# Kernel tuning notes

Measured on AMD Instinct MI355X. Metric: run time of the kernel, lower is better.

The kernel has to match this reference:

```python
import jax, jax.numpy as jnp
import jax.scipy.linalg as jsl
import numpy as np

EPS = 1e-6          # config.eps
MIN_EIG = 1e-4      # config.min_eigenvalue
B, N, K = 2, 2048, 3


def _so3_generators():
    # standard so(3) basis: [G_c]_{kl} = -eps_{ckl}
    G = np.zeros((3, 3, 3), np.float32)
    G[0, 1, 2] = -1.0; G[0, 2, 1] = 1.0
    G[1, 0, 2] = 1.0;  G[1, 2, 0] = -1.0
    G[2, 0, 1] = -1.0; G[2, 1, 0] = 1.0
    return jnp.asarray(G)


def _spd(key, b, n, k):
    # well-conditioned SPD covariances (as a real model would produce)
    A = jax.random.normal(key, (b, n, k, k), jnp.float32)
    return jnp.einsum('bnkl,bnml->bnkm', A, A) / k + 0.5 * jnp.eye(k, dtype=jnp.float32)


def setup_inputs() -> dict:
    key = jax.random.key(0)
    k0, k1, k2, k3 = jax.random.split(key, 4)
    Sigma_prior = _spd(k0, B, N, K)
    Sigma_q = _spd(k1, B, N, K)
    phi = jax.random.normal(k2, (B, N, K), jnp.float32)          # gauge field, C == K == 3
    beta = jax.random.uniform(k3, (B, N, N), jnp.float32) / N    # attention-like weights, rows O(1)
    return {
        'Sigma_prior': Sigma_prior,
        'Sigma_q': Sigma_q,
        'phi': phi,
        'beta': beta,
        'generators': _so3_generators(),
    }


def _batched_expm(mats):
    # mats: (B, N, K, K) -> elementwise matrix exponential
    b, n, k, _ = mats.shape
    return jax.vmap(jsl.expm)(mats.reshape(-1, k, k)).reshape(b, n, k, k)


def reference(Sigma_prior, Sigma_q, phi, beta, generators):
    b, n, k, _ = Sigma_prior.shape
    I = jnp.eye(k, dtype=Sigma_prior.dtype)

    # precisions (regularized inverses)
    Lambda_p = jnp.linalg.inv(Sigma_prior + EPS * I)   # (B,N,K,K)
    Lambda_q = jnp.linalg.inv(Sigma_q + EPS * I)       # (B,N,K,K)

    # gauge transport Omega_ij = e^{phi_i} e^{-phi_j}
    phi_mat = jnp.einsum('bnc,ckl->bnkl', phi, generators)
    exp_phi = _batched_expm(phi_mat)
    exp_neg_phi = _batched_expm(-phi_mat)
    Omega = jnp.einsum('bikl,bjlm->bijkm', exp_phi, exp_neg_phi)   # (B,N,N,K,K)

    # transported neighbor precision: Omega Lambda_q Omega^T
    Lt = jnp.einsum('bijkl,bjlm,bijnm->bijkn', Omega, Lambda_q, Omega)

    # incoming social term: sum_j beta_ij * Lt_ij
    M_in = jnp.einsum('bij,bijkl->bikl', beta, Lt)

    # outgoing recoil: (sum_j beta_ji) * Lambda_q_i
    M_out = beta.sum(axis=1)[..., None, None] * Lambda_q

    M = Lambda_p + M_in + M_out
    M = 0.5 * (M + jnp.swapaxes(M, -1, -2))

    # eigenvalue floor + inverse via eigh
    w, V = jnp.linalg.eigh(M)
    w = jnp.maximum(w, MIN_EIG)
    M_pd = jnp.einsum('bnkl,bnl,bnml->bnkm', V, w, V)
    M_inv = jnp.einsum('bnkl,bnl,bnml->bnkm', V, 1.0 / w, V)
    return M_pd, M_inv
```

## Files before the change

### kernel.cpp

```cpp
#include <hip/hip_runtime.h>
#include <math.h>

#define EPS_REG 1e-6f
#define MIN_EIG_F 1e-4f
#define RB 8


__device__ __forceinline__ void sym_inv3(const float m[3][3], float o[3][3]) {
    float c00 = m[1][1]*m[2][2] - m[1][2]*m[2][1];
    float c01 = m[1][2]*m[2][0] - m[1][0]*m[2][2];
    float c02 = m[1][0]*m[2][1] - m[1][1]*m[2][0];
    float det = m[0][0]*c00 + m[0][1]*c01 + m[0][2]*c02;
    float inv = 1.0f / det;
    o[0][0] = c00*inv;
    o[1][0] = c01*inv;
    o[2][0] = c02*inv;
    o[0][1] = (m[0][2]*m[2][1]-m[0][1]*m[2][2])*inv;
    o[1][1] = (m[0][0]*m[2][2]-m[0][2]*m[2][0])*inv;
    o[2][1] = (m[0][1]*m[2][0]-m[0][0]*m[2][1])*inv;
    o[0][2] = (m[0][1]*m[1][2]-m[0][2]*m[1][1])*inv;
    o[1][2] = (m[0][2]*m[1][0]-m[0][0]*m[1][2])*inv;
    o[2][2] = (m[0][0]*m[1][1]-m[0][1]*m[1][0])*inv;
}

__device__ __forceinline__ void rodrigues(float w0, float w1, float w2, float R[3][3]) {
    float th2 = w0*w0 + w1*w1 + w2*w2;
    float th = sqrtf(th2);
    float a, b;
    if (th < 1e-4f) { a = 1.0f - th2*(1.0f/6.0f); b = 0.5f - th2*(1.0f/24.0f); }
    else            { a = sinf(th)/th;            b = (1.0f - cosf(th))/th2; }
    R[0][0] = 1.0f + b*(w0*w0 - th2); R[0][1] = -a*w2 + b*w0*w1;        R[0][2] =  a*w1 + b*w0*w2;
    R[1][0] =  a*w2 + b*w0*w1;        R[1][1] = 1.0f + b*(w1*w1 - th2); R[1][2] = -a*w0 + b*w1*w2;
    R[2][0] = -a*w1 + b*w0*w2;        R[2][1] =  a*w0 + b*w1*w2;        R[2][2] = 1.0f + b*(w2*w2 - th2);
}

__device__ __forceinline__ void jrot(float A[3][3], float V[3][3], int p, int q) {
    float apq = A[p][q];
    if (fabsf(apq) < 1e-20f) return;
    float theta = (A[q][q] - A[p][p]) / (2.0f * apq);
    float t = 1.0f / (fabsf(theta) + sqrtf(1.0f + theta*theta));
    if (theta < 0.0f) t = -t;
    float c = 1.0f / sqrtf(1.0f + t*t);
    float s = t * c;
    int r = 3 - p - q;
    float apq_t = t*apq;
    A[p][p] -= apq_t;
    A[q][q] += apq_t;
    A[p][q] = 0.0f; A[q][p] = 0.0f;
    float arp = A[r][p], arq = A[r][q];
    A[r][p] = c*arp - s*arq; A[p][r] = A[r][p];
    A[r][q] = s*arp + c*arq; A[q][r] = A[r][q];
    #pragma unroll
    for (int k = 0; k < 3; k++) {
        float vkp = V[k][p], vkq = V[k][q];
        V[k][p] = c*vkp - s*vkq;
        V[k][q] = s*vkp + c*vkq;
    }
}

__global__ __launch_bounds__(64) void precompute_S_kernel(
        const float* __restrict__ Sq,
        const float* __restrict__ phi,
        float* __restrict__ S,
        int BN) {
    __shared__ float sq_s[576];
    __shared__ float ph_s[192];
    __shared__ float so_s[384];
    int tid = threadIdx.x;
    int p0 = blockIdx.x * 64;

    const float4* src = (const float4*)(Sq + (size_t)p0 * 9);
    #pragma unroll
    for (int i = tid; i < 144; i += 64) ((float4*)sq_s)[i] = src[i];
    const float4* psrc = (const float4*)(phi + (size_t)p0 * 3);
    if (tid < 48) ((float4*)ph_s)[tid] = psrc[tid];
    __syncthreads();

    float m[3][3], lq[3][3];
    #pragma unroll
    for (int i = 0; i < 3; i++)
        #pragma unroll
        for (int j = 0; j < 3; j++) m[i][j] = sq_s[tid*9 + i*3 + j];
    m[0][0] += EPS_REG; m[1][1] += EPS_REG; m[2][2] += EPS_REG;
    sym_inv3(m, lq);

    float R[3][3];
    rodrigues(ph_s[tid*3], ph_s[tid*3+1], ph_s[tid*3+2], R);

    float U[3][3];
    #pragma unroll
    for (int i = 0; i < 3; i++)
        #pragma unroll
        for (int j = 0; j < 3; j++)
            U[i][j] = lq[i][0]*R[0][j] + lq[i][1]*R[1][j] + lq[i][2]*R[2][j];
    float s00 = R[0][0]*U[0][0] + R[1][0]*U[1][0] + R[2][0]*U[2][0];
    float s01 = R[0][0]*U[0][1] + R[1][0]*U[1][1] + R[2][0]*U[2][1];
    float s02 = R[0][0]*U[0][2] + R[1][0]*U[1][2] + R[2][0]*U[2][2];
    float s11 = R[0][1]*U[0][1] + R[1][1]*U[1][1] + R[2][1]*U[2][1];
    float s12 = R[0][1]*U[0][2] + R[1][1]*U[1][2] + R[2][1]*U[2][2];
    float s22 = R[0][2]*U[0][2] + R[1][2]*U[1][2] + R[2][2]*U[2][2];
    so_s[tid*6+0]=s00; so_s[tid*6+1]=s01; so_s[tid*6+2]=s02;
    so_s[tid*6+3]=s11; so_s[tid*6+4]=s12; so_s[tid*6+5]=s22;
    __syncthreads();
    float4* dst = (float4*)(S + (size_t)p0 * 6);
    #pragma unroll
    for (int i = tid; i < 96; i += 64) dst[i] = ((float4*)so_s)[i];
}

__global__ __launch_bounds__(256) void fused_beta_kernel(
        const float* __restrict__ beta,
        const float* __restrict__ S,
        float* __restrict__ T,
        float* __restrict__ partial,
        int B, int N) {
    int tid = threadIdx.x;
    int grow0 = blockIdx.x * RB;
    int b = grow0 / N;
    int chunksPerB = N / RB;
    int chunk = (grow0 - b * N) / RB;
    const float* sb = S + (size_t)b * N * 6;

    float acc[RB][6];
    #pragma unroll
    for (int r = 0; r < RB; r++)
        #pragma unroll
        for (int c = 0; c < 6; c++) acc[r][c] = 0.0f;

    int jtiles = N / 1024;
    for (int jt = 0; jt < jtiles; jt++) {
        int c0 = jt * 1024 + 4 * tid;
        float4 s4[6];
        const float4* sp = (const float4*)(sb + (size_t)c0 * 6);
        #pragma unroll
        for (int u = 0; u < 6; u++) s4[u] = sp[u];
        const float* sv = (const float*)s4;

        float csum0 = 0.f, csum1 = 0.f, csum2 = 0.f, csum3 = 0.f;
        #pragma unroll
        for (int r = 0; r < RB; r++) {
            float4 w4 = *(const float4*)(beta + (size_t)(grow0 + r) * N + c0);
            csum0 += w4.x; csum1 += w4.y; csum2 += w4.z; csum3 += w4.w;
            #pragma unroll
            for (int c = 0; c < 6; c++) {
                acc[r][c] += w4.x * sv[0*6 + c];
                acc[r][c] += w4.y * sv[1*6 + c];
                acc[r][c] += w4.z * sv[2*6 + c];
                acc[r][c] += w4.w * sv[3*6 + c];
            }
        }
        *(float4*)(partial + ((size_t)b * chunksPerB + chunk) * N + c0) =
            make_float4(csum0, csum1, csum2, csum3);
    }

    __shared__ float red[256][49];
    __shared__ float red2[4][48];
    #pragma unroll
    for (int r = 0; r < RB; r++)
        #pragma unroll
        for (int c = 0; c < 6; c++)
            red[tid][r * 6 + c] = acc[r][c];
    __syncthreads();
    if (tid < 192) {
        int v = tid % 48, grp = tid / 48;
        float s = 0.0f;
        #pragma unroll 8
        for (int r = 0; r < 64; r++) s += red[grp * 64 + r][v];
        red2[grp][v] = s;
    }
    __syncthreads();
    if (tid < 48) {
        float v = red2[0][tid] + red2[1][tid] + red2[2][tid] + red2[3][tid];
        T[(size_t)grow0 * 6 + tid] = v;
    }
}

__global__ __launch_bounds__(256) void finalize_kernel(
        const float* __restrict__ Sp,
        const float* __restrict__ Sq,
        const float* __restrict__ phi,
        const float* __restrict__ T,
        const float* __restrict__ partial,
        float* __restrict__ out,
        int B, int N) {
    int tid  = threadIdx.x;
    int lane = tid & 63;
    int sub  = tid >> 6;
    int p0   = blockIdx.x * 64;
    int BN   = B * N;
    int b    = p0 / N;
    int i0   = p0 - b * N;
    int chunks = N / RB;

    __shared__ float redc[4][64];
    __shared__ float sp_s[576], sq_s[576], ph_s[192], t_s[384];
    __shared__ float o1_s[576], o2_s[576];

    int cpg = chunks / 4;
    float csp = 0.0f;
    const float* pp = partial + ((size_t)b * chunks + sub * cpg) * N + (i0 + lane);
    #pragma unroll 8
    for (int c = 0; c < cpg; c++) { csp += *pp; pp += (size_t)N; }
    redc[sub][lane] = csp;

    {
        const float4* s1 = (const float4*)(Sp + (size_t)p0 * 9);
        const float4* s2 = (const float4*)(Sq + (size_t)p0 * 9);
        if (tid < 144) { ((float4*)sp_s)[tid] = s1[tid]; ((float4*)sq_s)[tid] = s2[tid]; }
        const float4* s3 = (const float4*)(phi + (size_t)p0 * 3);
        if (tid < 48) ((float4*)ph_s)[tid] = s3[tid];
        const float4* s4 = (const float4*)(T + (size_t)p0 * 6);
        if (tid < 96) ((float4*)t_s)[tid] = s4[tid];
    }
    __syncthreads();

    if (tid < 64) {
        float cs = redc[0][lane] + redc[1][lane] + redc[2][lane] + redc[3][lane];

        float m[3][3], lp[3][3], lq[3][3];
        #pragma unroll
        for (int i = 0; i < 3; i++)
            #pragma unroll
            for (int j = 0; j < 3; j++) m[i][j] = sq_s[lane*9 + i*3 + j];
        m[0][0] += EPS_REG; m[1][1] += EPS_REG; m[2][2] += EPS_REG;
        sym_inv3(m, lq);
        #pragma unroll
        for (int i = 0; i < 3; i++)
            #pragma unroll
            for (int j = 0; j < 3; j++) m[i][j] = sp_s[lane*9 + i*3 + j];
        m[0][0] += EPS_REG; m[1][1] += EPS_REG; m[2][2] += EPS_REG;
        sym_inv3(m, lp);

        float R[3][3];
        rodrigues(ph_s[lane*3], ph_s[lane*3+1], ph_s[lane*3+2], R);

        const float* tp = t_s + lane * 6;
        float Tm[3][3] = {{tp[0],tp[1],tp[2]},{tp[1],tp[3],tp[4]},{tp[2],tp[4],tp[5]}};

        float U[3][3], M[3][3];
        #pragma unroll
        for (int ii = 0; ii < 3; ii++)
            #pragma unroll
            for (int jj = 0; jj < 3; jj++)
                U[ii][jj] = R[ii][0]*Tm[0][jj] + R[ii][1]*Tm[1][jj] + R[ii][2]*Tm[2][jj];
        #pragma unroll
        for (int ii = 0; ii < 3; ii++)
            #pragma unroll
            for (int jj = 0; jj < 3; jj++) {
                float min_ij = U[ii][0]*R[jj][0] + U[ii][1]*R[jj][1] + U[ii][2]*R[jj][2];
                M[ii][jj] = lp[ii][jj] + min_ij + cs * lq[ii][jj];
            }
        float A[3][3];
        #pragma unroll
        for (int ii = 0; ii < 3; ii++)
            #pragma unroll
            for (int jj = 0; jj < 3; jj++) A[ii][jj] = 0.5f * (M[ii][jj] + M[jj][ii]);

        float V[3][3] = {{1,0,0},{0,1,0},{0,0,1}};
        #pragma unroll
        for (int sweep = 0; sweep < 6; sweep++) {
            jrot(A, V, 0, 1);
            jrot(A, V, 0, 2);
            jrot(A, V, 1, 2);
        }
        float w0 = fmaxf(A[0][0], MIN_EIG_F);
        float w1 = fmaxf(A[1][1], MIN_EIG_F);
        float w2 = fmaxf(A[2][2], MIN_EIG_F);
        float iw0 = 1.0f/w0, iw1 = 1.0f/w1, iw2 = 1.0f/w2;

        #pragma unroll
        for (int ii = 0; ii < 3; ii++)
            #pragma unroll
            for (int jj = 0; jj < 3; jj++) {
                o1_s[lane*9 + ii*3 + jj] = V[ii][0]*w0*V[jj][0] + V[ii][1]*w1*V[jj][1] + V[ii][2]*w2*V[jj][2];
                o2_s[lane*9 + ii*3 + jj] = V[ii][0]*iw0*V[jj][0] + V[ii][1]*iw1*V[jj][1] + V[ii][2]*iw2*V[jj][2];
            }
    }
    __syncthreads();

    float4* d1 = (float4*)(out + (size_t)p0 * 9);
    float4* d2 = (float4*)(out + (size_t)BN * 9 + (size_t)p0 * 9);
    if (tid < 144) { d1[tid] = ((float4*)o1_s)[tid]; d2[tid] = ((float4*)o2_s)[tid]; }
}

extern "C" void kernel_launch(void* const* d_in, const int* in_sizes, int n_in,
                              void* d_out, int out_size, void* d_ws, size_t ws_size,
                              hipStream_t stream) {
    const float* Sp   = (const float*)d_in[0];
    const float* Sq   = (const float*)d_in[1];
    const float* phi  = (const float*)d_in[2];
    const float* beta = (const float*)d_in[3];

    int BN = in_sizes[2] / 3;
    int N  = (int)((long long)in_sizes[3] / BN);
    int B  = BN / N;

    float* ws = (float*)d_ws;
    float* S  = ws;
    float* T  = S + (size_t)BN * 6;
    float* partial = T + (size_t)BN * 6;

    float* outf = (float*)d_out;

    precompute_S_kernel<<<BN / 64, 64, 0, stream>>>(Sq, phi, S, BN);

    fused_beta_kernel<<<BN / RB, 256, 0, stream>>>(beta, S, T, partial, B, N);

    finalize_kernel<<<BN / 64, 256, 0, stream>>>(Sp, Sq, phi, T, partial, outf, B, N);
}
```

Baseline: 26.95 us.

## Fuse S precompute into beta reduction kernel, recomputing S per block in LDS

Removes the separate precompute_S kernel launch. Each beta block now recomputes all N transported precisions for its batch into shared memory (SoA layout) and reads them from LDS instead of global memory. The first tile of beta rows is prefetched before that compute so the load latency overlaps it, and the reduction buffer reuses the same shared memory. The cost is redundant computation: every one of the 512 blocks does 2048 3x3 inversions and Rodrigues evaluations, so the same work is repeated many times over.

After: 29.88 us. +10.9%, slower.

```diff
diff --git a/kernel.cpp b/kernel.cpp
--- a/kernel.cpp
+++ b/kernel.cpp
@@ -58,67 +58,69 @@
     }
 }
 
-__global__ __launch_bounds__(64) void precompute_S_kernel(
+__device__ __forceinline__ void compute_S_point(const float* __restrict__ sq9,
+                                                const float* __restrict__ ph3,
+                                                float sv[6]) {
+    float m[3][3], lq[3][3];
+    #pragma unroll
+    for (int i = 0; i < 3; i++)
+        #pragma unroll
+        for (int j = 0; j < 3; j++) m[i][j] = sq9[i*3 + j];
+    m[0][0] += EPS_REG; m[1][1] += EPS_REG; m[2][2] += EPS_REG;
+    sym_inv3(m, lq);
+    float R[3][3];
+    rodrigues(ph3[0], ph3[1], ph3[2], R);
+    float U[3][3];
+    #pragma unroll
+    for (int i = 0; i < 3; i++)
+        #pragma unroll
+        for (int j = 0; j < 3; j++)
+            U[i][j] = lq[i][0]*R[0][j] + lq[i][1]*R[1][j] + lq[i][2]*R[2][j];
+    sv[0] = R[0][0]*U[0][0] + R[1][0]*U[1][0] + R[2][0]*U[2][0];
+    sv[1] = R[0][0]*U[0][1] + R[1][0]*U[1][1] + R[2][0]*U[2][1];
+    sv[2] = R[0][0]*U[0][2] + R[1][0]*U[1][2] + R[2][0]*U[2][2];
+    sv[3] = R[0][1]*U[0][1] + R[1][1]*U[1][1] + R[2][1]*U[2][1];
+    sv[4] = R[0][1]*U[0][2] + R[1][1]*U[1][2] + R[2][1]*U[2][2];
+    sv[5] = R[0][2]*U[0][2] + R[1][2]*U[1][2] + R[2][2]*U[2][2];
+}
+
+__global__ __launch_bounds__(256) void mega_beta_kernel(
         const float* __restrict__ Sq,
         const float* __restrict__ phi,
-        float* __restrict__ S,
-        int BN) {
-    __shared__ float sq_s[576];
-    __shared__ float ph_s[192];
-    __shared__ float so_s[384];
-    int tid = threadIdx.x;
-    int p0 = blockIdx.x * 64;
-
-    const float4* src = (const float4*)(Sq + (size_t)p0 * 9);
-    #pragma unroll
-    for (int i = tid; i < 144; i += 64) ((float4*)sq_s)[i] = src[i];
-    const float4* psrc = (const float4*)(phi + (size_t)p0 * 3);
-    if (tid < 48) ((float4*)ph_s)[tid] = psrc[tid];
-    __syncthreads();
-
-    float m[3][3], lq[3][3];
-    #pragma unroll
-    for (int i = 0; i < 3; i++)
-        #pragma unroll
-        for (int j = 0; j < 3; j++) m[i][j] = sq_s[tid*9 + i*3 + j];
-    m[0][0] += EPS_REG; m[1][1] += EPS_REG; m[2][2] += EPS_REG;
-    sym_inv3(m, lq);
-
-    float R[3][3];
-    rodrigues(ph_s[tid*3], ph_s[tid*3+1], ph_s[tid*3+2], R);
-
-    float U[3][3];
-    #pragma unroll
-    for (int i = 0; i < 3; i++)
-        #pragma unroll
-        for (int j = 0; j < 3; j++)
-            U[i][j] = lq[i][0]*R[0][j] + lq[i][1]*R[1][j] + lq[i][2]*R[2][j];
-    float s00 = R[0][0]*U[0][0] + R[1][0]*U[1][0] + R[2][0]*U[2][0];
-    float s01 = R[0][0]*U[0][1] + R[1][0]*U[1][1] + R[2][0]*U[2][1];
-    float s02 = R[0][0]*U[0][2] + R[1][0]*U[1][2] + R[2][0]*U[2][2];
-    float s11 = R[0][1]*U[0][1] + R[1][1]*U[1][1] + R[2][1]*U[2][1];
-    float s12 = R[0][1]*U[0][2] + R[1][1]*U[1][2] + R[2][1]*U[2][2];
-    float s22 = R[0][2]*U[0][2] + R[1][2]*U[1][2] + R[2][2]*U[2][2];
-    so_s[tid*6+0]=s00; so_s[tid*6+1]=s01; so_s[tid*6+2]=s02;
-    so_s[tid*6+3]=s11; so_s[tid*6+4]=s12; so_s[tid*6+5]=s22;
-    __syncthreads();
-    float4* dst = (float4*)(S + (size_t)p0 * 6);
-    #pragma unroll
-    for (int i = tid; i < 96; i += 64) dst[i] = ((float4*)so_s)[i];
-}
-
-__global__ __launch_bounds__(256) void fused_beta_kernel(
         const float* __restrict__ beta,
-        const float* __restrict__ S,
         float* __restrict__ T,
         float* __restrict__ partial,
         int B, int N) {
+    __shared__ float smem[12288];
+    __shared__ float red2[4][48];
+
     int tid = threadIdx.x;
     int grow0 = blockIdx.x * RB;
     int b = grow0 / N;
     int chunksPerB = N / RB;
     int chunk = (grow0 - b * N) / RB;
-    const float* sb = S + (size_t)b * N * 6;
+
+    float4 pre[RB];
+    {
+        int c0 = 4 * tid;
+        #pragma unroll
+        for (int r = 0; r < RB; r++)
+            pre[r] = *(const float4*)(beta + (size_t)(grow0 + r) * N + c0);
+    }
+
+    {
+        const float* sqb = Sq  + (size_t)b * N * 9;
+        const float* phb = phi + (size_t)b * N * 3;
+        int npts = N / 256;
+        for (int ph = 0; ph < npts; ph++) {
+            int p = ph * 256 + tid;
+            float sv[6];
+            compute_S_point(sqb + (size_t)p * 9, phb + (size_t)p * 3, sv);
+            #pragma unroll
+            for (int c = 0; c < 6; c++) smem[c * 2048 + p] = sv[c];
+        }
+    }
+    __syncthreads();
 
     float acc[RB][6];
     #pragma unroll
@@ -129,42 +131,42 @@
     int jtiles = N / 1024;
     for (int jt = 0; jt < jtiles; jt++) {
         int c0 = jt * 1024 + 4 * tid;
-        float4 s4[6];
-        const float4* sp = (const float4*)(sb + (size_t)c0 * 6);
-        #pragma unroll
-        for (int u = 0; u < 6; u++) s4[u] = sp[u];
-        const float* sv = (const float*)s4;
+        float4 s0 = *(const float4*)&smem[0*2048 + c0];
+        float4 s1 = *(const float4*)&smem[1*2048 + c0];
+        float4 s2 = *(const float4*)&smem[2*2048 + c0];
+        float4 s3 = *(const float4*)&smem[3*2048 + c0];
+        float4 s4v = *(const float4*)&smem[4*2048 + c0];
+        float4 s5 = *(const float4*)&smem[5*2048 + c0];
 
         float csum0 = 0.f, csum1 = 0.f, csum2 = 0.f, csum3 = 0.f;
         #pragma unroll
         for (int r = 0; r < RB; r++) {
-            float4 w4 = *(const float4*)(beta + (size_t)(grow0 + r) * N + c0);
+            float4 w4 = (jt == 0) ? pre[r]
+                      : *(const float4*)(beta + (size_t)(grow0 + r) * N + c0);
             csum0 += w4.x; csum1 += w4.y; csum2 += w4.z; csum3 += w4.w;
-            #pragma unroll
-            for (int c = 0; c < 6; c++) {
-                acc[r][c] += w4.x * sv[0*6 + c];
-                acc[r][c] += w4.y * sv[1*6 + c];
-                acc[r][c] += w4.z * sv[2*6 + c];
-                acc[r][c] += w4.w * sv[3*6 + c];
-            }
+            acc[r][0] += w4.x*s0.x + w4.y*s0.y + w4.z*s0.z + w4.w*s0.w;
+            acc[r][1] += w4.x*s1.x + w4.y*s1.y + w4.z*s1.z + w4.w*s1.w;
+            acc[r][2] += w4.x*s2.x + w4.y*s2.y + w4.z*s2.z + w4.w*s2.w;
+            acc[r][3] += w4.x*s3.x + w4.y*s3.y + w4.z*s3.z + w4.w*s3.w;
+            acc[r][4] += w4.x*s4v.x + w4.y*s4v.y + w4.z*s4v.z + w4.w*s4v.w;
+            acc[r][5] += w4.x*s5.x + w4.y*s5.y + w4.z*s5.z + w4.w*s5.w;
         }
         *(float4*)(partial + ((size_t)b * chunksPerB + chunk) * N + c0) =
             make_float4(csum0, csum1, csum2, csum3);
     }
-
-    __shared__ float red[256][49];
-    __shared__ float red2[4][48];
+    __syncthreads();
+
     #pragma unroll
     for (int r = 0; r < RB; r++)
         #pragma unroll
         for (int c = 0; c < 6; c++)
-            red[tid][r * 6 + c] = acc[r][c];
+            smem[tid * 48 + r * 6 + c] = acc[r][c];
     __syncthreads();
     if (tid < 192) {
         int v = tid % 48, grp = tid / 48;
         float s = 0.0f;
         #pragma unroll 8
-        for (int r = 0; r < 64; r++) s += red[grp * 64 + r][v];
+        for (int r = 0; r < 64; r++) s += smem[(grp * 64 + r) * 48 + v];
         red2[grp][v] = s;
     }
     __syncthreads();
@@ -295,15 +297,12 @@
     int B  = BN / N;
 
     float* ws = (float*)d_ws;
-    float* S  = ws;
-    float* T  = S + (size_t)BN * 6;
+    float* T  = ws;
     float* partial = T + (size_t)BN * 6;
 
     float* outf = (float*)d_out;
 
-    precompute_S_kernel<<<BN / 64, 64, 0, stream>>>(Sq, phi, S, BN);
-
-    fused_beta_kernel<<<BN / RB, 256, 0, stream>>>(beta, S, T, partial, B, N);
+    mega_beta_kernel<<<BN / RB, 256, 0, stream>>>(Sq, phi, beta, T, partial, B, N);
 
     finalize_kernel<<<BN / 64, 256, 0, stream>>>(Sp, Sq, phi, T, partial, outf, B, N);
 }
```

## Store transported precisions as SoA planes and halve finalize block size

Applied to the files above, without the earlier changes.

The precompute kernel now writes the six symmetric components of each transported precision as separate planes (structure-of-arrays) instead of interleaved 6-float records. The beta reduction kernel therefore loads one float4 per component across four consecutive columns, which simplifies the FMA pattern. The finalize kernel now handles 32 points per block with 8 groups doing the column-sum reduction, doubling the block count. The shared reduction array loses its padding column, which may introduce bank conflicts.

New measurement: 27.31 us. Within noise of the previous version (+1.3%).

```diff
diff --git a/kernel.cpp b/kernel.cpp
--- a/kernel.cpp
+++ b/kernel.cpp
@@ -61,11 +61,10 @@
 __global__ __launch_bounds__(64) void precompute_S_kernel(
         const float* __restrict__ Sq,
         const float* __restrict__ phi,
-        float* __restrict__ S,
+        float* __restrict__ Splanes,
         int BN) {
     __shared__ float sq_s[576];
     __shared__ float ph_s[192];
-    __shared__ float so_s[384];
     int tid = threadIdx.x;
     int p0 = blockIdx.x * 64;
 
@@ -93,32 +92,29 @@
         #pragma unroll
         for (int j = 0; j < 3; j++)
             U[i][j] = lq[i][0]*R[0][j] + lq[i][1]*R[1][j] + lq[i][2]*R[2][j];
-    float s00 = R[0][0]*U[0][0] + R[1][0]*U[1][0] + R[2][0]*U[2][0];
-    float s01 = R[0][0]*U[0][1] + R[1][0]*U[1][1] + R[2][0]*U[2][1];
-    float s02 = R[0][0]*U[0][2] + R[1][0]*U[1][2] + R[2][0]*U[2][2];
-    float s11 = R[0][1]*U[0][1] + R[1][1]*U[1][1] + R[2][1]*U[2][1];
-    float s12 = R[0][1]*U[0][2] + R[1][1]*U[1][2] + R[2][1]*U[2][2];
-    float s22 = R[0][2]*U[0][2] + R[1][2]*U[1][2] + R[2][2]*U[2][2];
-    so_s[tid*6+0]=s00; so_s[tid*6+1]=s01; so_s[tid*6+2]=s02;
-    so_s[tid*6+3]=s11; so_s[tid*6+4]=s12; so_s[tid*6+5]=s22;
-    __syncthreads();
-    float4* dst = (float4*)(S + (size_t)p0 * 6);
-    #pragma unroll
-    for (int i = tid; i < 96; i += 64) dst[i] = ((float4*)so_s)[i];
+    float sv[6];
+    sv[0] = R[0][0]*U[0][0] + R[1][0]*U[1][0] + R[2][0]*U[2][0];
+    sv[1] = R[0][0]*U[0][1] + R[1][0]*U[1][1] + R[2][0]*U[2][1];
+    sv[2] = R[0][0]*U[0][2] + R[1][0]*U[1][2] + R[2][0]*U[2][2];
+    sv[3] = R[0][1]*U[0][1] + R[1][1]*U[1][1] + R[2][1]*U[2][1];
+    sv[4] = R[0][1]*U[0][2] + R[1][1]*U[1][2] + R[2][1]*U[2][2];
+    sv[5] = R[0][2]*U[0][2] + R[1][2]*U[1][2] + R[2][2]*U[2][2];
+    #pragma unroll
+    for (int c = 0; c < 6; c++)
+        Splanes[(size_t)c * BN + p0 + tid] = sv[c];
 }
 
 __global__ __launch_bounds__(256) void fused_beta_kernel(
         const float* __restrict__ beta,
-        const float* __restrict__ S,
+        const float* __restrict__ Splanes,
         float* __restrict__ T,
         float* __restrict__ partial,
-        int B, int N) {
+        int B, int N, int BN) {
     int tid = threadIdx.x;
     int grow0 = blockIdx.x * RB;
     int b = grow0 / N;
     int chunksPerB = N / RB;
     int chunk = (grow0 - b * N) / RB;
-    const float* sb = S + (size_t)b * N * 6;
 
     float acc[RB][6];
     #pragma unroll
@@ -129,11 +125,10 @@
     int jtiles = N / 1024;
     for (int jt = 0; jt < jtiles; jt++) {
         int c0 = jt * 1024 + 4 * tid;
-        float4 s4[6];
-        const float4* sp = (const float4*)(sb + (size_t)c0 * 6);
-        #pragma unroll
-        for (int u = 0; u < 6; u++) s4[u] = sp[u];
-        const float* sv = (const float*)s4;
+        float4 s[6];
+        #pragma unroll
+        for (int c = 0; c < 6; c++)
+            s[c] = *(const float4*)(Splanes + (size_t)c * BN + (size_t)b * N + c0);
 
         float csum0 = 0.f, csum1 = 0.f, csum2 = 0.f, csum3 = 0.f;
         #pragma unroll
@@ -141,18 +136,14 @@
             float4 w4 = *(const float4*)(beta + (size_t)(grow0 + r) * N + c0);
             csum0 += w4.x; csum1 += w4.y; csum2 += w4.z; csum3 += w4.w;
             #pragma unroll
-            for (int c = 0; c < 6; c++) {
-                acc[r][c] += w4.x * sv[0*6 + c];
-                acc[r][c] += w4.y * sv[1*6 + c];
-                acc[r][c] += w4.z * sv[2*6 + c];
-                acc[r][c] += w4.w * sv[3*6 + c];
-            }
+            for (int c = 0; c < 6; c++)
+                acc[r][c] += w4.x*s[c].x + w4.y*s[c].y + w4.z*s[c].z + w4.w*s[c].w;
         }
         *(float4*)(partial + ((size_t)b * chunksPerB + chunk) * N + c0) =
             make_float4(csum0, csum1, csum2, csum3);
     }
 
-    __shared__ float red[256][49];
+    __shared__ float red[256][48];
     __shared__ float red2[4][48];
     #pragma unroll
     for (int r = 0; r < RB; r++)
@@ -182,58 +173,60 @@
         const float* __restrict__ partial,
         float* __restrict__ out,
         int B, int N) {
-    int tid  = threadIdx.x;
-    int lane = tid & 63;
-    int sub  = tid >> 6;
-    int p0   = blockIdx.x * 64;
+    int tid   = threadIdx.x;
+    int lane32 = tid & 31;
+    int grp    = tid >> 5;
+    int p0   = blockIdx.x * 32;
     int BN   = B * N;
     int b    = p0 / N;
     int i0   = p0 - b * N;
     int chunks = N / RB;
 
-    __shared__ float redc[4][64];
-    __shared__ float sp_s[576], sq_s[576], ph_s[192], t_s[384];
-    __shared__ float o1_s[576], o2_s[576];
-
-    int cpg = chunks / 4;
+    __shared__ float redc[8][32];
+    __shared__ float sp_s[288], sq_s[288], ph_s[96], t_s[192];
+    __shared__ float o1_s[288], o2_s[288];
+
+    int cpg = chunks / 8;
     float csp = 0.0f;
-    const float* pp = partial + ((size_t)b * chunks + sub * cpg) * N + (i0 + lane);
+    const float* pp = partial + ((size_t)b * chunks + grp * cpg) * N + (i0 + lane32);
     #pragma unroll 8
     for (int c = 0; c < cpg; c++) { csp += *pp; pp += (size_t)N; }
-    redc[sub][lane] = csp;
+    redc[grp][lane32] = csp;
 
     {
         const float4* s1 = (const float4*)(Sp + (size_t)p0 * 9);
         const float4* s2 = (const float4*)(Sq + (size_t)p0 * 9);
-        if (tid < 144) { ((float4*)sp_s)[tid] = s1[tid]; ((float4*)sq_s)[tid] = s2[tid]; }
+        if (tid < 72) { ((float4*)sp_s)[tid] = s1[tid]; ((float4*)sq_s)[tid] = s2[tid]; }
         const float4* s3 = (const float4*)(phi + (size_t)p0 * 3);
-        if (tid < 48) ((float4*)ph_s)[tid] = s3[tid];
+        if (tid < 24) ((float4*)ph_s)[tid] = s3[tid];
         const float4* s4 = (const float4*)(T + (size_t)p0 * 6);
-        if (tid < 96) ((float4*)t_s)[tid] = s4[tid];
-    }
-    __syncthreads();
-
-    if (tid < 64) {
-        float cs = redc[0][lane] + redc[1][lane] + redc[2][lane] + redc[3][lane];
+        if (tid < 48) ((float4*)t_s)[tid] = s4[tid];
+    }
+    __syncthreads();
+
+    if (tid < 32) {
+        float cs = 0.0f;
+        #pragma unroll
+        for (int g = 0; g < 8; g++) cs += redc[g][tid];
 
         float m[3][3], lp[3][3], lq[3][3];
         #pragma unroll
         for (int i = 0; i < 3; i++)
             #pragma unroll
-            for (int j = 0; j < 3; j++) m[i][j] = sq_s[lane*9 + i*3 + j];
+            for (int j = 0; j < 3; j++) m[i][j] = sq_s[tid*9 + i*3 + j];
         m[0][0] += EPS_REG; m[1][1] += EPS_REG; m[2][2] += EPS_REG;
         sym_inv3(m, lq);
         #pragma unroll
         for (int i = 0; i < 3; i++)
             #pragma unroll
-            for (int j = 0; j < 3; j++) m[i][j] = sp_s[lane*9 + i*3 + j];
+            for (int j = 0; j < 3; j++) m[i][j] = sp_s[tid*9 + i*3 + j];
         m[0][0] += EPS_REG; m[1][1] += EPS_REG; m[2][2] += EPS_REG;
         sym_inv3(m, lp);
 
         float R[3][3];
-        rodrigues(ph_s[lane*3], ph_s[lane*3+1], ph_s[lane*3+2], R);
-
-        const float* tp = t_s + lane * 6;
+        rodrigues(ph_s[tid*3], ph_s[tid*3+1], ph_s[tid*3+2], R);
+
+        const float* tp = t_s + tid * 6;
         float Tm[3][3] = {{tp[0],tp[1],tp[2]},{tp[1],tp[3],tp[4]},{tp[2],tp[4],tp[5]}};
 
         float U[3][3], M[3][3];
@@ -271,15 +264,15 @@
         for (int ii = 0; ii < 3; ii++)
             #pragma unroll
             for (int jj = 0; jj < 3; jj++) {
-                o1_s[lane*9 + ii*3 + jj] = V[ii][0]*w0*V[jj][0] + V[ii][1]*w1*V[jj][1] + V[ii][2]*w2*V[jj][2];
-                o2_s[lane*9 + ii*3 + jj] = V[ii][0]*iw0*V[jj][0] + V[ii][1]*iw1*V[jj][1] + V[ii][2]*iw2*V[jj][2];
+                o1_s[tid*9 + ii*3 + jj] = V[ii][0]*w0*V[jj][0] + V[ii][1]*w1*V[jj][1] + V[ii][2]*w2*V[jj][2];
+                o2_s[tid*9 + ii*3 + jj] = V[ii][0]*iw0*V[jj][0] + V[ii][1]*iw1*V[jj][1] + V[ii][2]*iw2*V[jj][2];
             }
     }
     __syncthreads();
 
     float4* d1 = (float4*)(out + (size_t)p0 * 9);
     float4* d2 = (float4*)(out + (size_t)BN * 9 + (size_t)p0 * 9);
-    if (tid < 144) { d1[tid] = ((float4*)o1_s)[tid]; d2[tid] = ((float4*)o2_s)[tid]; }
+    if (tid < 72) { d1[tid] = ((float4*)o1_s)[tid]; d2[tid] = ((float4*)o2_s)[tid]; }
 }
 
 extern "C" void kernel_launch(void* const* d_in, const int* in_sizes, int n_in,
@@ -295,15 +288,15 @@
     int B  = BN / N;
 
     float* ws = (float*)d_ws;
-    float* S  = ws;
-    float* T  = S + (size_t)BN * 6;
+    float* Splanes = ws;
+    float* T       = Splanes + (size_t)BN * 6;
     float* partial = T + (size_t)BN * 6;
 
     float* outf = (float*)d_out;
 
-    precompute_S_kernel<<<BN / 64, 64, 0, stream>>>(Sq, phi, S, BN);
-
-    fused_beta_kernel<<<BN / RB, 256, 0, stream>>>(beta, S, T, partial, B, N);
-
-    finalize_kernel<<<BN / 64, 256, 0, stream>>>(Sp, Sq, phi, T, partial, outf, B, N);
-}
+    precompute_S_kernel<<<BN / 64, 64, 0, stream>>>(Sq, phi, Splanes, BN);
+
+    fused_beta_kernel<<<BN / RB, 256, 0, stream>>>(beta, Splanes, T, partial, B, N, BN);
+
+    finalize_kernel<<<BN / 32, 256, 0, stream>>>(Sp, Sq, phi, T, partial, outf, B, N);
+}
```
